# Performance work log

Hardware: AMD Instinct MI355X
Metric: run time of the kernel (lower is better)

The kernel has to match this reference:

```python
import jax, jax.numpy as jnp
import numpy as np

H = 256  # hidden_dim
Z = 4    # z_dim

def gru_step(x, h, Wih, Whh, bih, bhh):
    gi = x @ Wih.T + bih            # [B, 3H]
    gh = h @ Whh.T + bhh            # [B, 3H]
    ir, iz, inn = jnp.split(gi, 3, axis=-1)
    hr, hz, hn = jnp.split(gh, 3, axis=-1)
    r = jax.nn.sigmoid(ir + hr)
    z = jax.nn.sigmoid(iz + hz)
    n = jnp.tanh(inn + r * hn)
    return (1.0 - z) * n + z * h

def gru_scan(xs, h0, Wih, Whh, bih, bhh):
    # xs: [L, B, D] time-major; returns all hidden states [L, B, H]
    def step(h, x):
        h = gru_step(x, h, Wih, Whh, bih, bhh)
        return h, h
    _, hs = jax.lax.scan(step, h0, xs)
    return hs

def feat_z(z, fz_W1, fz_b1, fz_W2, fz_b2):
    # MLPEmbedding(z_dim -> [z_dim//2] -> feature_z), Linear+tanh per layer (dropout off in eval)
    h = jnp.tanh(z @ fz_W1.T + fz_b1)
    return jnp.tanh(h @ fz_W2.T + fz_b2)

def _make_params(key):
    ks = jax.random.split(key, 32)
    s = 0.05
    p = {}
    p['fx_W'] = jax.random.normal(ks[0], (64, 1)) * s
    p['fx_b'] = jnp.zeros((64,))
    p['fz_W1'] = jax.random.normal(ks[1], (2, 4)) * s
    p['fz_b1'] = jnp.zeros((2,))
    p['fz_W2'] = jax.random.normal(ks[2], (32, 2)) * s
    p['fz_b2'] = jnp.zeros((32,))
    p['phi1_Wih'] = jax.random.normal(ks[3], (3 * H, 64)) * s
    p['phi1_Whh'] = jax.random.normal(ks[4], (3 * H, H)) * s
    p['phi1_bih'] = jnp.zeros((3 * H,))
    p['phi1_bhh'] = jnp.zeros((3 * H,))
    p['phi2_Wih'] = jax.random.normal(ks[5], (3 * H, 32)) * s
    p['phi2_Whh'] = jax.random.normal(ks[6], (3 * H, H)) * s
    p['phi2_bih'] = jnp.zeros((3 * H,))
    p['phi2_bhh'] = jnp.zeros((3 * H,))
    p['pn_locW'] = jax.random.normal(ks[7], (Z, 2 * H)) * s
    p['pn_locb'] = jnp.zeros((Z,))
    p['pn_scaleW'] = jax.random.normal(ks[8], (Z, 2 * H)) * s
    p['pn_scaleb'] = jnp.zeros((Z,))
    p['th_Wih'] = jax.random.normal(ks[9], (3 * H, 32)) * s
    p['th_Whh'] = jax.random.normal(ks[10], (3 * H, H)) * s
    p['th_bih'] = jnp.zeros((3 * H,))
    p['th_bhh'] = jnp.zeros((3 * H,))
    p['tn_locW'] = jax.random.normal(ks[11], (1, H)) * s
    p['tn_locb'] = jnp.zeros((1,))
    return p

def setup_inputs() -> dict:
    key = jax.random.key(0)
    kx, ke, kp = jax.random.split(key, 3)
    B, L = 256, 512
    inp = {
        'x': jax.random.normal(kx, (B, L, 1), dtype=jnp.float32),
        'eps': jax.random.normal(ke, (L, B, Z), dtype=jnp.float32),
    }
    inp.update(_make_params(kp))
    return inp

def reference(x, eps, fx_W, fx_b, fz_W1, fz_b1, fz_W2, fz_b2,
              phi1_Wih, phi1_Whh, phi1_bih, phi1_bhh,
              phi2_Wih, phi2_Whh, phi2_bih, phi2_bhh,
              pn_locW, pn_locb, pn_scaleW, pn_scaleb,
              th_Wih, th_Whh, th_bih, th_bhh,
              tn_locW, tn_locb):
    B, L, _ = x.shape
    # ---- encode ----
    xf = jnp.tanh(x @ fx_W.T + fx_b)                 # [B, L, 64] feature_extra_x
    xs_rev = jnp.transpose(xf[:, ::-1, :], (1, 0, 2))  # [L, B, 64] reversed, time-major
    h0 = jnp.zeros((B, H), dtype=x.dtype)
    xh = gru_scan(xs_rev, h0, phi1_Wih, phi1_Whh, phi1_bih, phi1_bhh)  # [L, B, H]
    xh_r = xh[::-1]                                  # flip back to forward time order

    def enc_step(carry, inp_t):
        zh, zf = carry
        xh_t, eps_t = inp_t
        zh = gru_step(zf, zh, phi2_Wih, phi2_Whh, phi2_bih, phi2_bhh)
        cat = jnp.concatenate([zh, xh_t], axis=-1)   # [B, 2H]
        z_loc = cat @ pn_locW.T + pn_locb
        z_scale = jax.nn.softplus(cat @ pn_scaleW.T + pn_scaleb)
        z_t = z_loc + z_scale * eps_t                # Normal sample (n_sample=1 -> mean == sample)
        zf = feat_z(z_t, fz_W1, fz_b1, fz_W2, fz_b2)
        return (zh, zf), z_t

    zf0 = jnp.zeros((B, 32), dtype=x.dtype)
    _, z_tm = jax.lax.scan(enc_step, (h0, zf0), (xh_r, eps))  # [L, B, Z]

    # ---- decode ----
    zf_seq = feat_z(z_tm, fz_W1, fz_b1, fz_W2, fz_b2)          # [L, B, 32]
    hs = gru_scan(zf_seq, h0, th_Wih, th_Whh, th_bih, th_bhh)  # [L, B, H]
    x_loc = hs @ tn_locW.T + tn_locb                           # [L, B, 1]
    return jnp.transpose(x_loc, (1, 0, 2))                     # [B, L, 1]
```

## Files before the change

### kernel.cpp

```cpp
#include <hip/hip_runtime.h>
#include <hip/hip_bf16.h>
#include <stdint.h>


struct RvaeParams {
  const float *x, *eps;
  const float *fx_W, *fx_b;
  const float *fz_W1, *fz_b1, *fz_W2, *fz_b2;
  const float *p1_Wih, *p1_Whh, *p1_bih, *p1_bhh;
  const float *p2_Wih, *p2_Whh, *p2_bih, *p2_bhh;
  const float *pn_locW, *pn_locb, *pn_scaleW, *pn_scaleb;
  const float *th_Wih, *th_Whh, *th_bih, *th_bhh;
  const float *tn_locW, *tn_locb;
  float* out;
  unsigned* ctr;
  float* hbuf;
  float* zpart;
  float* zf_seq;
  __hip_bfloat16* xh;
};

__device__ __forceinline__ float agent_load_f32(const float* p) {
  return __hip_atomic_load(p, __ATOMIC_RELAXED, __HIP_MEMORY_SCOPE_AGENT);
}
__device__ __forceinline__ void agent_store_f32(float* p, float v) {
  __hip_atomic_store(p, v, __ATOMIC_RELAXED, __HIP_MEMORY_SCOPE_AGENT);
}
__device__ __forceinline__ unsigned long long agent_load_u64(const unsigned long long* p) {
  return __hip_atomic_load(p, __ATOMIC_RELAXED, __HIP_MEMORY_SCOPE_AGENT);
}
__device__ __forceinline__ float sigm(float xx) { return 1.0f / (1.0f + __expf(-xx)); }
__device__ __forceinline__ float ftanh(float xx) { return 1.0f - 2.0f / (__expf(2.0f * xx) + 1.0f); }
__device__ __forceinline__ float softplusf(float xx) { return (xx > 15.0f) ? xx : log1pf(__expf(xx)); }

__device__ __forceinline__ void gh_part(const float* Wh, const float* hL, int b, int u,
                                        float& ar, float& az, float& an) {
  float r0 = 0.f, z0 = 0.f, n0 = 0.f;
  const float4* h4 = (const float4*)hL + b * 65;
  const float4* wr = (const float4*)Wh + u * 65;
  const float4* wz = (const float4*)Wh + (32 + u) * 65;
  const float4* wn = (const float4*)Wh + (64 + u) * 65;
#pragma unroll 4
  for (int k = 0; k < 64; ++k) {
    float4 hv = h4[k];
    float4 a = wr[k]; float4 c = wz[k]; float4 d = wn[k];
    r0 = fmaf(a.x, hv.x, r0); r0 = fmaf(a.y, hv.y, r0); r0 = fmaf(a.z, hv.z, r0); r0 = fmaf(a.w, hv.w, r0);
    z0 = fmaf(c.x, hv.x, z0); z0 = fmaf(c.y, hv.y, z0); z0 = fmaf(c.z, hv.z, z0); z0 = fmaf(c.w, hv.w, z0);
    n0 = fmaf(d.x, hv.x, n0); n0 = fmaf(d.y, hv.y, n0); n0 = fmaf(d.z, hv.z, n0); n0 = fmaf(d.w, hv.w, n0);
  }
  ar = r0; az = z0; an = n0;
}

template<int KD4>
__device__ __forceinline__ void gi_part(const float* Wi, int strideF4, const float* inL, int b, int u,
                                        float& gr, float& gz, float& gn) {
  float r0 = 0.f, z0 = 0.f, n0 = 0.f;
  const float4* i4 = (const float4*)inL + b * 17;
  const float4* wr = (const float4*)Wi + u * strideF4;
  const float4* wz = (const float4*)Wi + (32 + u) * strideF4;
  const float4* wn = (const float4*)Wi + (64 + u) * strideF4;
#pragma unroll 4
  for (int k = 0; k < KD4; ++k) {
    float4 hv = i4[k];
    float4 a = wr[k]; float4 c = wz[k]; float4 d = wn[k];
    r0 = fmaf(a.x, hv.x, r0); r0 = fmaf(a.y, hv.y, r0); r0 = fmaf(a.z, hv.z, r0); r0 = fmaf(a.w, hv.w, r0);
    z0 = fmaf(c.x, hv.x, z0); z0 = fmaf(c.y, hv.y, z0); z0 = fmaf(c.z, hv.z, z0); z0 = fmaf(c.w, hv.w, z0);
    n0 = fmaf(d.x, hv.x, n0); n0 = fmaf(d.y, hv.y, n0); n0 = fmaf(d.z, hv.z, n0); n0 = fmaf(d.w, hv.w, n0);
  }
  gr = r0; gz = z0; gn = n0;
}

extern "C" __global__ void __launch_bounds__(256, 1) rvae_main(RvaeParams P) {
  __shared__ __align__(16) float Wh[96 * 260];
  __shared__ __align__(16) float SB[7584];
  __shared__ __align__(16) float hL[8 * 260];
  __shared__ __align__(16) float inL[8 * 68];
  __shared__ float bihL[96], bhhL[96];
  __shared__ float fxwL[64], fxbL[64];
  __shared__ float fzW1L[8], fzb1L[2], fzW2L[64], fzb2L[32];
  __shared__ float pnlb[4], pnsb[4];
  __shared__ float wred[4 * 8 * 8];
  __shared__ float zred[64];
  __shared__ float ztL[32];
  __shared__ float hmL[16];
  __shared__ float oredL[4 * 8];
  __shared__ float tnwL[32];
  __shared__ unsigned bcount;

  const int tid = threadIdx.x;
  const int wgid = blockIdx.x;
  const int s = wgid >> 5;
  const int g = wgid & 31;
  const int b_l = tid & 7;
  const int u = tid >> 3;
  const int j = s * 32 + u;
  const int bg = g * 8 + b_l;
  unsigned* gctr = P.ctr + g * 16;

  if (tid < 64) { fxwL[tid] = P.fx_W[tid]; fxbL[tid] = P.fx_b[tid]; fzW2L[tid] = P.fz_W2[tid]; }
  if (tid < 8)  fzW1L[tid] = P.fz_W1[tid];
  if (tid < 2)  fzb1L[tid] = P.fz_b1[tid];
  if (tid < 32) fzb2L[tid] = P.fz_b2[tid];
  if (tid < 4)  { pnlb[tid] = P.pn_locb[tid]; pnsb[tid] = P.pn_scaleb[tid]; }
  if (tid == 0) bcount = 0;

  auto gbar = [&]() {
    __syncthreads();
    if (tid == 0) {
      unsigned target = (++bcount) * 8u;
      __hip_atomic_fetch_add(gctr, 1u, __ATOMIC_RELEASE, __HIP_MEMORY_SCOPE_AGENT);
      int guard = 0;
      while (__hip_atomic_load(gctr, __ATOMIC_ACQUIRE, __HIP_MEMORY_SCOPE_AGENT) < target) {
        __builtin_amdgcn_s_sleep(1);
        if (++guard > (1 << 27)) break;
      }
    }
    __syncthreads();
  };

  auto load_whh = [&](const float* Whh) {
    for (int rr = 0; rr < 96; ++rr) {
      int gate = rr >> 5, uu = rr & 31;
      Wh[rr * 260 + tid] = Whh[(gate * 256 + s * 32 + uu) * 256 + tid];
    }
  };
  auto load_wih32 = [&](const float* Wih) {
    for (int blk = 0; blk < 12; ++blk) {
      int rr = blk * 8 + (tid >> 5); int c = tid & 31;
      int gate = rr >> 5, uu = rr & 31;
      SB[rr * 36 + c] = Wih[(gate * 256 + s * 32 + uu) * 32 + c];
    }
  };
  auto load_bias = [&](const float* bih, const float* bhh) {
    if (tid < 96) {
      int gate = tid >> 5, uu = tid & 31;
      bihL[tid] = bih[gate * 256 + s * 32 + uu];
      bhhL[tid] = bhh[gate * 256 + s * 32 + uu];
    }
  };

  load_whh(P.p1_Whh);
  for (int blk = 0; blk < 24; ++blk) {
    int rr = blk * 4 + (tid >> 6); int c = tid & 63;
    int gate = rr >> 5, uu = rr & 31;
    SB[rr * 68 + c] = P.p1_Wih[(gate * 256 + s * 32 + uu) * 64 + c];
  }
  load_bias(P.p1_bih, P.p1_bhh);
  agent_store_f32(P.hbuf + bg * 256 + j, 0.0f);
  {
#pragma unroll
    for (int i = 0; i < 2; ++i) {
      int idx = tid + i * 256; int bb = idx >> 6, k = idx & 63;
      float xv = P.x[(size_t)(g * 8 + bb) * 512 + 511];
      inL[bb * 68 + k] = ftanh(fmaf(xv, fxwL[k], fxbL[k]));
    }
  }
  gbar();
  for (int t = 0; t < 512; ++t) {
    const float* hin = P.hbuf + (t & 1) * 65536 + g * 2048;
    float* hout = P.hbuf + ((t + 1) & 1) * 65536;
    unsigned long long hv[4];
    const unsigned long long* h64 = (const unsigned long long*)hin;
#pragma unroll
    for (int i = 0; i < 4; ++i) hv[i] = agent_load_u64(h64 + tid + i * 256);
    float gr, gz, gn;
    gi_part<16>(SB, 17, inL, b_l, u, gr, gz, gn);
#pragma unroll
    for (int i = 0; i < 4; ++i) {
      int idx = tid + i * 256; int bb = idx >> 7, kp = (idx & 127) * 2;
      union { unsigned long long q; float f[2]; } cv; cv.q = hv[i];
      hL[bb * 260 + kp] = cv.f[0]; hL[bb * 260 + kp + 1] = cv.f[1];
    }
    __syncthreads();
    float ar, az, an;
    gh_part(Wh, hL, b_l, u, ar, az, an);
    float hold = hL[b_l * 260 + j];
    float r = sigm(gr + bihL[u] + ar + bhhL[u]);
    float z = sigm(gz + bihL[32 + u] + az + bhhL[32 + u]);
    float n = ftanh(fmaf(r, an + bhhL[64 + u], gn + bihL[64 + u]));
    float hnew = fmaf(z, hold - n, n);
    int t_in = 511 - t;
    agent_store_f32(hout + bg * 256 + j, hnew);
    P.xh[((size_t)wgid * 512 + t_in) * 256 + b_l * 32 + u] = __float2bfloat16(hnew);
    if (t < 511) {
#pragma unroll
      for (int i = 0; i < 2; ++i) {
        int idx = tid + i * 256; int bb = idx >> 6, k = idx & 63;
        float xv = P.x[(size_t)(g * 8 + bb) * 512 + (t_in - 1)];
        inL[bb * 68 + k] = ftanh(fmaf(xv, fxwL[k], fxbL[k]));
      }
    }
    gbar();
  }

  __syncthreads();
  load_whh(P.p2_Whh);
  load_wih32(P.p2_Wih);
  for (int idx = tid; idx < 2048; idx += 256) {
    int o = idx >> 9, c = idx & 511;
    SB[3456 + o * 516 + c] = P.pn_locW[idx];
    SB[5520 + o * 516 + c] = P.pn_scaleW[idx];
  }
  load_bias(P.p2_bih, P.p2_bhh);
  agent_store_f32(P.hbuf + bg * 256 + j, 0.0f);
  for (int idx = tid; idx < 8 * 68; idx += 256) inL[idx] = 0.0f;
  gbar();
  for (int t = 0; t < 512; ++t) {
    const float* hin = P.hbuf + (t & 1) * 65536 + g * 2048;
    float* hout = P.hbuf + ((t + 1) & 1) * 65536;
    unsigned long long hv[4];
    const unsigned long long* h64 = (const unsigned long long*)hin;
#pragma unroll
    for (int i = 0; i < 4; ++i) hv[i] = agent_load_u64(h64 + tid + i * 256);
    float xhv = __bfloat162float(P.xh[((size_t)wgid * 512 + t) * 256 + b_l * 32 + u]);
    float gr, gz, gn;
    gi_part<8>(SB, 9, inL, b_l, u, gr, gz, gn);
#pragma unroll
    for (int i = 0; i < 4; ++i) {
      int idx = tid + i * 256; int bb = idx >> 7, kp = (idx & 127) * 2;
      union { unsigned long long q; float f[2]; } cv; cv.q = hv[i];
      hL[bb * 260 + kp] = cv.f[0]; hL[bb * 260 + kp + 1] = cv.f[1];
    }
    __syncthreads();
    float ar, az, an;
    gh_part(Wh, hL, b_l, u, ar, az, an);
    float hold = hL[b_l * 260 + j];
    float r = sigm(gr + bihL[u] + ar + bhhL[u]);
    float z = sigm(gz + bihL[32 + u] + az + bhhL[32 + u]);
    float n = ftanh(fmaf(r, an + bhhL[64 + u], gn + bihL[64 + u]));
    float hnew = fmaf(z, hold - n, n);
    agent_store_f32(hout + bg * 256 + j, hnew);
    float p[8];
#pragma unroll
    for (int o = 0; o < 4; ++o)
      p[o] = fmaf(hnew, SB[3456 + o * 516 + j], xhv * SB[3456 + o * 516 + 256 + j]);
#pragma unroll
    for (int o = 0; o < 4; ++o)
      p[4 + o] = fmaf(hnew, SB[5520 + o * 516 + j], xhv * SB[5520 + o * 516 + 256 + j]);
#pragma unroll
    for (int o = 0; o < 8; ++o) {
      float v = p[o];
      v += __shfl_down(v, 32); v += __shfl_down(v, 16); v += __shfl_down(v, 8);
      p[o] = v;
    }
    {
      int lane = tid & 63, wv = tid >> 6;
      if (lane < 8) {
#pragma unroll
        for (int o = 0; o < 8; ++o) wred[wv * 64 + lane * 8 + o] = p[o];
      }
    }
    __syncthreads();
    float* zp = P.zpart + (t & 1) * 16384 + g * 512;
    if (tid < 64) {
      int bb = tid >> 3, o = tid & 7;
      float sum = wred[bb * 8 + o] + wred[64 + bb * 8 + o] + wred[128 + bb * 8 + o] + wred[192 + bb * 8 + o];
      agent_store_f32(zp + s * 64 + bb * 8 + o, sum);
    }
    gbar();
    if (tid < 64) {
      int bb = tid >> 3, o = tid & 7;
      float sum = 0.f;
#pragma unroll
      for (int sp = 0; sp < 8; ++sp) sum += agent_load_f32(zp + sp * 64 + bb * 8 + o);
      zred[bb * 8 + o] = sum;
    }
    __syncthreads();
    if (tid < 32) {
      int bb = tid >> 2, zi = tid & 3;
      float loc = zred[bb * 8 + zi] + pnlb[zi];
      float sc = softplusf(zred[bb * 8 + 4 + zi] + pnsb[zi]);
      float e = P.eps[((size_t)t * 256 + g * 8 + bb) * 4 + zi];
      ztL[bb * 4 + zi] = fmaf(sc, e, loc);
    }
    __syncthreads();
    if (tid < 16) {
      int bb = tid >> 1, m = tid & 1;
      float a = fzb1L[m];
#pragma unroll
      for (int i = 0; i < 4; ++i) a = fmaf(ztL[bb * 4 + i], fzW1L[m * 4 + i], a);
      hmL[bb * 2 + m] = ftanh(a);
    }
    __syncthreads();
    {
      int bb = tid >> 5, o = tid & 31;
      float zf = ftanh(fmaf(hmL[bb * 2], fzW2L[o * 2], fmaf(hmL[bb * 2 + 1], fzW2L[o * 2 + 1], fzb2L[o])));
      inL[bb * 68 + o] = zf;
      if (s == 0) agent_store_f32(P.zf_seq + ((size_t)t * 256 + g * 8 + bb) * 32 + o, zf);
    }
    __syncthreads();
  }

  __syncthreads();
  load_whh(P.th_Whh);
  load_wih32(P.th_Wih);
  load_bias(P.th_bih, P.th_bhh);
  if (tid < 32) tnwL[tid] = P.tn_locW[s * 32 + tid];
  agent_store_f32(P.hbuf + bg * 256 + j, 0.0f);
  gbar();
  const float tnb = P.tn_locb[0];
  for (int t = 0; t < 512; ++t) {
    const float* hin = P.hbuf + (t & 1) * 65536 + g * 2048;
    float* hout = P.hbuf + ((t + 1) & 1) * 65536;
    unsigned long long hv[4];
    const unsigned long long* h64 = (const unsigned long long*)hin;
#pragma unroll
    for (int i = 0; i < 4; ++i) hv[i] = agent_load_u64(h64 + tid + i * 256);
    {
      int bb = tid >> 5, o = tid & 31;
      inL[bb * 68 + o] = agent_load_f32(P.zf_seq + ((size_t)t * 256 + g * 8 + bb) * 32 + o);
    }
#pragma unroll
    for (int i = 0; i < 4; ++i) {
      int idx = tid + i * 256; int bb = idx >> 7, kp = (idx & 127) * 2;
      union { unsigned long long q; float f[2]; } cv; cv.q = hv[i];
      hL[bb * 260 + kp] = cv.f[0]; hL[bb * 260 + kp + 1] = cv.f[1];
    }
    __syncthreads();
    float gr, gz, gn;
    gi_part<8>(SB, 9, inL, b_l, u, gr, gz, gn);
    float ar, az, an;
    gh_part(Wh, hL, b_l, u, ar, az, an);
    float hold = hL[b_l * 260 + j];
    float r = sigm(gr + bihL[u] + ar + bhhL[u]);
    float z = sigm(gz + bihL[32 + u] + az + bhhL[32 + u]);
    float n = ftanh(fmaf(r, an + bhhL[64 + u], gn + bihL[64 + u]));
    float hnew = fmaf(z, hold - n, n);
    agent_store_f32(hout + bg * 256 + j, hnew);
    float pv = hnew * tnwL[u];
    pv += __shfl_down(pv, 32); pv += __shfl_down(pv, 16); pv += __shfl_down(pv, 8);
    {
      int lane = tid & 63, wv = tid >> 6;
      if (lane < 8) oredL[wv * 8 + lane] = pv;
    }
    __syncthreads();
    if (tid < 8) {
      float v = oredL[tid] + oredL[8 + tid] + oredL[16 + tid] + oredL[24 + tid];
      if (s == 0) v += tnb;
      atomicAdd(P.out + (size_t)(g * 8 + tid) * 512 + t, v);
    }
    gbar();
  }
}

extern "C" void kernel_launch(void* const* d_in, const int* in_sizes, int n_in,
                              void* d_out, int out_size, void* d_ws, size_t ws_size,
                              hipStream_t stream) {
  (void)in_sizes; (void)n_in; (void)ws_size;
  RvaeParams P;
  P.x        = (const float*)d_in[0];
  P.eps      = (const float*)d_in[1];
  P.fx_W     = (const float*)d_in[2];  P.fx_b     = (const float*)d_in[3];
  P.fz_W1    = (const float*)d_in[4];  P.fz_b1    = (const float*)d_in[5];
  P.fz_W2    = (const float*)d_in[6];  P.fz_b2    = (const float*)d_in[7];
  P.p1_Wih   = (const float*)d_in[8];  P.p1_Whh   = (const float*)d_in[9];
  P.p1_bih   = (const float*)d_in[10]; P.p1_bhh   = (const float*)d_in[11];
  P.p2_Wih   = (const float*)d_in[12]; P.p2_Whh   = (const float*)d_in[13];
  P.p2_bih   = (const float*)d_in[14]; P.p2_bhh   = (const float*)d_in[15];
  P.pn_locW  = (const float*)d_in[16]; P.pn_locb  = (const float*)d_in[17];
  P.pn_scaleW= (const float*)d_in[18]; P.pn_scaleb= (const float*)d_in[19];
  P.th_Wih   = (const float*)d_in[20]; P.th_Whh   = (const float*)d_in[21];
  P.th_bih   = (const float*)d_in[22]; P.th_bhh   = (const float*)d_in[23];
  P.tn_locW  = (const float*)d_in[24]; P.tn_locb  = (const float*)d_in[25];
  P.out = (float*)d_out;
  char* ws = (char*)d_ws;
  P.ctr    = (unsigned*)ws;
  P.hbuf   = (float*)(ws + 4096);
  P.zpart  = (float*)(ws + 4096 + 524288);
  P.zf_seq = (float*)(ws + 4096 + 524288 + 131072);
  P.xh = (__hip_bfloat16*)(ws + 4096 + 524288 + 131072 + 16777216);

  hipMemsetAsync(d_out, 0, (size_t)out_size * sizeof(float), stream);
  hipMemsetAsync(d_ws, 0, 4096, stream);
  void* args[] = { (void*)&P };
  hipError_t err = hipLaunchCooperativeKernel((void*)rvae_main, dim3(256), dim3(256), args, 0, stream);
  if (err != hipSuccess) {
    hipLaunchKernelGGL(rvae_main, dim3(256), dim3(256), 0, stream, P);
  }
}
```

Before: 12.78 ms.

## Keep GRU recurrent weights in registers with split-K DPP reduction, 512 threads

Moves each block's slice of the recurrent Whh (and Wih) weights out of LDS and into per-thread registers. Each thread now handles 16 input columns for one hidden unit across all 8 batch rows, and the partial sums are combined with DPP row reductions. Blocks grow to 512 threads so the dot-product work is spread over more lanes and LDS weight traffic per step goes away. In exchange it needs a lot of registers per thread, adds a shuffle reduction and an extra LDS stage (gsum) each step, and adds a padding array that looks meant to shape LDS allocation or occupancy.

```diff
diff --git a/kernel.cpp b/kernel.cpp
--- a/kernel.cpp
+++ b/kernel.cpp
@@ -29,80 +29,66 @@
 __device__ __forceinline__ unsigned long long agent_load_u64(const unsigned long long* p) {
   return __hip_atomic_load(p, __ATOMIC_RELAXED, __HIP_MEMORY_SCOPE_AGENT);
 }
-__device__ __forceinline__ float sigm(float xx) { return 1.0f / (1.0f + __expf(-xx)); }
-__device__ __forceinline__ float ftanh(float xx) { return 1.0f - 2.0f / (__expf(2.0f * xx) + 1.0f); }
-__device__ __forceinline__ float softplusf(float xx) { return (xx > 15.0f) ? xx : log1pf(__expf(xx)); }
-
-__device__ __forceinline__ void gh_part(const float* Wh, const float* hL, int b, int u,
-                                        float& ar, float& az, float& an) {
-  float r0 = 0.f, z0 = 0.f, n0 = 0.f;
-  const float4* h4 = (const float4*)hL + b * 65;
-  const float4* wr = (const float4*)Wh + u * 65;
-  const float4* wz = (const float4*)Wh + (32 + u) * 65;
-  const float4* wn = (const float4*)Wh + (64 + u) * 65;
-#pragma unroll 4
-  for (int k = 0; k < 64; ++k) {
-    float4 hv = h4[k];
-    float4 a = wr[k]; float4 c = wz[k]; float4 d = wn[k];
-    r0 = fmaf(a.x, hv.x, r0); r0 = fmaf(a.y, hv.y, r0); r0 = fmaf(a.z, hv.z, r0); r0 = fmaf(a.w, hv.w, r0);
-    z0 = fmaf(c.x, hv.x, z0); z0 = fmaf(c.y, hv.y, z0); z0 = fmaf(c.z, hv.z, z0); z0 = fmaf(c.w, hv.w, z0);
-    n0 = fmaf(d.x, hv.x, n0); n0 = fmaf(d.y, hv.y, n0); n0 = fmaf(d.z, hv.z, n0); n0 = fmaf(d.w, hv.w, n0);
-  }
-  ar = r0; az = z0; an = n0;
-}
-
-template<int KD4>
-__device__ __forceinline__ void gi_part(const float* Wi, int strideF4, const float* inL, int b, int u,
-                                        float& gr, float& gz, float& gn) {
-  float r0 = 0.f, z0 = 0.f, n0 = 0.f;
-  const float4* i4 = (const float4*)inL + b * 17;
-  const float4* wr = (const float4*)Wi + u * strideF4;
-  const float4* wz = (const float4*)Wi + (32 + u) * strideF4;
-  const float4* wn = (const float4*)Wi + (64 + u) * strideF4;
-#pragma unroll 4
-  for (int k = 0; k < KD4; ++k) {
-    float4 hv = i4[k];
-    float4 a = wr[k]; float4 c = wz[k]; float4 d = wn[k];
-    r0 = fmaf(a.x, hv.x, r0); r0 = fmaf(a.y, hv.y, r0); r0 = fmaf(a.z, hv.z, r0); r0 = fmaf(a.w, hv.w, r0);
-    z0 = fmaf(c.x, hv.x, z0); z0 = fmaf(c.y, hv.y, z0); z0 = fmaf(c.z, hv.z, z0); z0 = fmaf(c.w, hv.w, z0);
-    n0 = fmaf(d.x, hv.x, n0); n0 = fmaf(d.y, hv.y, n0); n0 = fmaf(d.z, hv.z, n0); n0 = fmaf(d.w, hv.w, n0);
-  }
-  gr = r0; gz = z0; gn = n0;
-}
-
-extern "C" __global__ void __launch_bounds__(256, 1) rvae_main(RvaeParams P) {
-  __shared__ __align__(16) float Wh[96 * 260];
-  __shared__ __align__(16) float SB[7584];
-  __shared__ __align__(16) float hL[8 * 260];
+__device__ __forceinline__ float sigm(float v) { return 1.0f / (1.0f + __expf(-v)); }
+__device__ __forceinline__ float ftanh(float v) { return 1.0f - 2.0f / (__expf(2.0f * v) + 1.0f); }
+__device__ __forceinline__ float softplusf(float v) { return (v > 15.0f) ? v : log1pf(__expf(v)); }
+
+template<int CTRL>
+__device__ __forceinline__ float dpp_add(float v) {
+  int x = __builtin_amdgcn_update_dpp(0, __float_as_int(v), CTRL, 0xf, 0xf, true);
+  return v + __int_as_float(x);
+}
+__device__ __forceinline__ float row_reduce16(float v) {
+  v = dpp_add<0x111>(v);
+  v = dpp_add<0x112>(v);
+  v = dpp_add<0x114>(v);
+  v = dpp_add<0x118>(v);
+  return v;
+}
+
+extern "C" __global__ void __launch_bounds__(512, 2) rvae_main(RvaeParams P) {
+  __shared__ __align__(16) float hL[8 * 320];
   __shared__ __align__(16) float inL[8 * 68];
+  __shared__ __align__(16) float gsum[8 * 132];
+  __shared__ __align__(16) float SB[2 * 4 * 516];
   __shared__ float bihL[96], bhhL[96];
   __shared__ float fxwL[64], fxbL[64];
   __shared__ float fzW1L[8], fzb1L[2], fzW2L[64], fzb2L[32];
   __shared__ float pnlb[4], pnsb[4];
-  __shared__ float wred[4 * 8 * 8];
+  __shared__ float wred[256];
   __shared__ float zred[64];
   __shared__ float ztL[32];
   __shared__ float hmL[16];
-  __shared__ float oredL[4 * 8];
+  __shared__ float oredL[32];
   __shared__ float tnwL[32];
   __shared__ unsigned bcount;
+  __shared__ float lds_pad[11776];
 
   const int tid = threadIdx.x;
   const int wgid = blockIdx.x;
   const int s = wgid >> 5;
   const int g = wgid & 31;
+  const int kap = tid & 15;
+  const int uu = tid >> 4;
   const int b_l = tid & 7;
-  const int u = tid >> 3;
-  const int j = s * 32 + u;
+  const int up = (tid >> 3) & 31;
+  const int j = s * 32 + up;
   const int bg = g * 8 + b_l;
   unsigned* gctr = P.ctr + g * 16;
 
   if (tid < 64) { fxwL[tid] = P.fx_W[tid]; fxbL[tid] = P.fx_b[tid]; fzW2L[tid] = P.fz_W2[tid]; }
   if (tid < 8)  fzW1L[tid] = P.fz_W1[tid];
   if (tid < 2)  fzb1L[tid] = P.fz_b1[tid];
-  if (tid < 32) fzb2L[tid] = P.fz_b2[tid];
+  if (tid < 32) { fzb2L[tid] = P.fz_b2[tid]; tnwL[tid] = P.tn_locW[s * 32 + tid]; }
   if (tid < 4)  { pnlb[tid] = P.pn_locb[tid]; pnsb[tid] = P.pn_scaleb[tid]; }
   if (tid == 0) bcount = 0;
+  lds_pad[tid] = (float)tid;
+  asm volatile("" : : "v"(lds_pad[tid]) : "memory");
+
+  float whr[16], whz[16], whn[16];
+  float wir[4], wiz[4], win[4];
+  float pr[8], pz[8], pni[8], pnh[8];
+  unsigned long long q0, q1;
 
   auto gbar = [&]() {
     __syncthreads();
@@ -118,132 +104,183 @@
     __syncthreads();
   };
 
-  auto load_whh = [&](const float* Whh) {
-    for (int rr = 0; rr < 96; ++rr) {
-      int gate = rr >> 5, uu = rr & 31;
-      Wh[rr * 260 + tid] = Whh[(gate * 256 + s * 32 + uu) * 256 + tid];
-    }
-  };
-  auto load_wih32 = [&](const float* Wih) {
-    for (int blk = 0; blk < 12; ++blk) {
-      int rr = blk * 8 + (tid >> 5); int c = tid & 31;
-      int gate = rr >> 5, uu = rr & 31;
-      SB[rr * 36 + c] = Wih[(gate * 256 + s * 32 + uu) * 32 + c];
-    }
+  auto load_whh_regs = [&](const float* Whh) {
+    const float* base = Whh + (size_t)(s * 32 + uu) * 256 + kap * 16;
+#pragma unroll
+    for (int c = 0; c < 4; ++c) {
+      float4 vr = *(const float4*)(base + c * 4);
+      float4 vz = *(const float4*)(base + 65536 + c * 4);
+      float4 vn = *(const float4*)(base + 131072 + c * 4);
+      whr[4*c+0]=vr.x; whr[4*c+1]=vr.y; whr[4*c+2]=vr.z; whr[4*c+3]=vr.w;
+      whz[4*c+0]=vz.x; whz[4*c+1]=vz.y; whz[4*c+2]=vz.z; whz[4*c+3]=vz.w;
+      whn[4*c+0]=vn.x; whn[4*c+1]=vn.y; whn[4*c+2]=vn.z; whn[4*c+3]=vn.w;
+    }
+  };
+  auto load_wih64_regs = [&](const float* Wih) {
+    const float* base = Wih + (size_t)(s * 32 + uu) * 64 + kap * 4;
+    float4 vr = *(const float4*)(base);
+    float4 vz = *(const float4*)(base + 16384);
+    float4 vn = *(const float4*)(base + 32768);
+    wir[0]=vr.x; wir[1]=vr.y; wir[2]=vr.z; wir[3]=vr.w;
+    wiz[0]=vz.x; wiz[1]=vz.y; wiz[2]=vz.z; wiz[3]=vz.w;
+    win[0]=vn.x; win[1]=vn.y; win[2]=vn.z; win[3]=vn.w;
+  };
+  auto load_wih32_regs = [&](const float* Wih) {
+    const float* base = Wih + (size_t)(s * 32 + uu) * 32 + kap * 2;
+    float2 vr = *(const float2*)(base);
+    float2 vz = *(const float2*)(base + 8192);
+    float2 vn = *(const float2*)(base + 16384);
+    wir[0]=vr.x; wir[1]=vr.y; wiz[0]=vz.x; wiz[1]=vz.y; win[0]=vn.x; win[1]=vn.y;
   };
   auto load_bias = [&](const float* bih, const float* bhh) {
     if (tid < 96) {
-      int gate = tid >> 5, uu = tid & 31;
-      bihL[tid] = bih[gate * 256 + s * 32 + uu];
-      bhhL[tid] = bhh[gate * 256 + s * 32 + uu];
-    }
-  };
-
-  load_whh(P.p1_Whh);
-  for (int blk = 0; blk < 24; ++blk) {
-    int rr = blk * 4 + (tid >> 6); int c = tid & 63;
-    int gate = rr >> 5, uu = rr & 31;
-    SB[rr * 68 + c] = P.p1_Wih[(gate * 256 + s * 32 + uu) * 64 + c];
-  }
+      int gate = tid >> 5, u2 = tid & 31;
+      bihL[tid] = bih[gate * 256 + s * 32 + u2];
+      bhhL[tid] = bhh[gate * 256 + s * 32 + u2];
+    }
+  };
+  auto load_h_issue = [&](int t) {
+    const unsigned long long* h64 =
+        (const unsigned long long*)(P.hbuf + (t & 1) * 65536 + g * 2048) + tid * 2;
+    q0 = agent_load_u64(h64);
+    q1 = agent_load_u64(h64 + 1);
+  };
+  auto stage_h = [&]() {
+    int bb = tid >> 6, k4 = tid & 63;
+    union { unsigned long long q[2]; float f[4]; } cv; cv.q[0] = q0; cv.q[1] = q1;
+    float* dst = hL + bb * 320 + (k4 >> 2) * 20 + (k4 & 3) * 4;
+    *(float4*)dst = make_float4(cv.f[0], cv.f[1], cv.f[2], cv.f[3]);
+  };
+  auto gh_accum = [&]() {
+#pragma unroll
+    for (int b = 0; b < 8; ++b) {
+      const float* hp = hL + b * 320 + kap * 20;
+      float4 hcv[4];
+      hcv[0] = *(const float4*)(hp);     hcv[1] = *(const float4*)(hp + 4);
+      hcv[2] = *(const float4*)(hp + 8); hcv[3] = *(const float4*)(hp + 12);
+      float r = pr[b], z = pz[b], n = pnh[b];
+#pragma unroll
+      for (int c = 0; c < 4; ++c) {
+        r = fmaf(whr[4*c+0], hcv[c].x, r); r = fmaf(whr[4*c+1], hcv[c].y, r);
+        r = fmaf(whr[4*c+2], hcv[c].z, r); r = fmaf(whr[4*c+3], hcv[c].w, r);
+        z = fmaf(whz[4*c+0], hcv[c].x, z); z = fmaf(whz[4*c+1], hcv[c].y, z);
+        z = fmaf(whz[4*c+2], hcv[c].z, z); z = fmaf(whz[4*c+3], hcv[c].w, z);
+        n = fmaf(whn[4*c+0], hcv[c].x, n); n = fmaf(whn[4*c+1], hcv[c].y, n);
+        n = fmaf(whn[4*c+2], hcv[c].z, n); n = fmaf(whn[4*c+3], hcv[c].w, n);
+      }
+      pr[b] = r; pz[b] = z; pnh[b] = n;
+    }
+  };
+  auto reduce_write = [&]() {
+#pragma unroll
+    for (int b = 0; b < 8; ++b) {
+      pr[b] = row_reduce16(pr[b]);  pz[b] = row_reduce16(pz[b]);
+      pni[b] = row_reduce16(pni[b]); pnh[b] = row_reduce16(pnh[b]);
+    }
+    if (kap == 15) {
+#pragma unroll
+      for (int b = 0; b < 8; ++b) {
+        gsum[b*132 + uu]      = pr[b];
+        gsum[b*132 + 32 + uu] = pz[b];
+        gsum[b*132 + 64 + uu] = pni[b];
+        gsum[b*132 + 96 + uu] = pnh[b];
+      }
+    }
+  };
+  auto pointwise_h = [&](int t) -> float {
+    float rr = sigm(gsum[b_l*132 + up]      + bihL[up]      + bhhL[up]);
+    float zz = sigm(gsum[b_l*132 + 32 + up] + bihL[32 + up] + bhhL[32 + up]);
+    float nn = ftanh(fmaf(rr, gsum[b_l*132 + 96 + up] + bhhL[64 + up],
+                              gsum[b_l*132 + 64 + up] + bihL[64 + up]));
+    float hold = hL[b_l*320 + ((j >> 4) * 20) + (j & 15)];
+    float hnew = fmaf(zz, hold - nn, nn);
+    agent_store_f32(P.hbuf + (((t + 1) & 1) * 65536) + bg * 256 + j, hnew);
+    return hnew;
+  };
+
+  load_whh_regs(P.p1_Whh);
+  load_wih64_regs(P.p1_Wih);
   load_bias(P.p1_bih, P.p1_bhh);
-  agent_store_f32(P.hbuf + bg * 256 + j, 0.0f);
+  if (tid < 256) agent_store_f32(P.hbuf + bg * 256 + j, 0.0f);
+  __syncthreads();
   {
-#pragma unroll
-    for (int i = 0; i < 2; ++i) {
-      int idx = tid + i * 256; int bb = idx >> 6, k = idx & 63;
-      float xv = P.x[(size_t)(g * 8 + bb) * 512 + 511];
+    int bb = tid >> 6, k = tid & 63;
+    float xv = P.x[(size_t)(g * 8 + bb) * 512 + 511];
+    inL[bb * 68 + k] = ftanh(fmaf(xv, fxwL[k], fxbL[k]));
+  }
+  gbar();
+#pragma unroll 1
+  for (int t = 0; t < 512; ++t) {
+    load_h_issue(t);
+#pragma unroll
+    for (int b = 0; b < 8; ++b) {
+      float4 iv = *(const float4*)(inL + b * 68 + kap * 4);
+      pr[b]  = fmaf(wir[0], iv.x, fmaf(wir[1], iv.y, fmaf(wir[2], iv.z, wir[3] * iv.w)));
+      pz[b]  = fmaf(wiz[0], iv.x, fmaf(wiz[1], iv.y, fmaf(wiz[2], iv.z, wiz[3] * iv.w)));
+      pni[b] = fmaf(win[0], iv.x, fmaf(win[1], iv.y, fmaf(win[2], iv.z, win[3] * iv.w)));
+      pnh[b] = 0.0f;
+    }
+    stage_h();
+    __syncthreads();
+    gh_accum();
+    reduce_write();
+    __syncthreads();
+    int t_in = 511 - t;
+    if (tid < 256) {
+      float hnew = pointwise_h(t);
+      P.xh[((size_t)wgid * 512 + t_in) * 256 + b_l * 32 + up] = __float2bfloat16(hnew);
+    }
+    if (t < 511) {
+      int bb = tid >> 6, k = tid & 63;
+      float xv = P.x[(size_t)(g * 8 + bb) * 512 + (t_in - 1)];
       inL[bb * 68 + k] = ftanh(fmaf(xv, fxwL[k], fxbL[k]));
     }
-  }
+    gbar();
+  }
+
+  load_whh_regs(P.p2_Whh);
+  load_wih32_regs(P.p2_Wih);
+  load_bias(P.p2_bih, P.p2_bhh);
+  for (int idx = tid; idx < 2048; idx += 512) {
+    int o = idx >> 9, c = idx & 511;
+    SB[o * 516 + c] = P.pn_locW[idx];
+    SB[2064 + o * 516 + c] = P.pn_scaleW[idx];
+  }
+  if (tid < 256) agent_store_f32(P.hbuf + bg * 256 + j, 0.0f);
+  for (int idx = tid; idx < 8 * 36; idx += 512) inL[idx] = 0.0f;
   gbar();
+#pragma unroll 1
   for (int t = 0; t < 512; ++t) {
-    const float* hin = P.hbuf + (t & 1) * 65536 + g * 2048;
-    float* hout = P.hbuf + ((t + 1) & 1) * 65536;
-    unsigned long long hv[4];
-    const unsigned long long* h64 = (const unsigned long long*)hin;
-#pragma unroll
-    for (int i = 0; i < 4; ++i) hv[i] = agent_load_u64(h64 + tid + i * 256);
-    float gr, gz, gn;
-    gi_part<16>(SB, 17, inL, b_l, u, gr, gz, gn);
-#pragma unroll
-    for (int i = 0; i < 4; ++i) {
-      int idx = tid + i * 256; int bb = idx >> 7, kp = (idx & 127) * 2;
-      union { unsigned long long q; float f[2]; } cv; cv.q = hv[i];
-      hL[bb * 260 + kp] = cv.f[0]; hL[bb * 260 + kp + 1] = cv.f[1];
-    }
-    __syncthreads();
-    float ar, az, an;
-    gh_part(Wh, hL, b_l, u, ar, az, an);
-    float hold = hL[b_l * 260 + j];
-    float r = sigm(gr + bihL[u] + ar + bhhL[u]);
-    float z = sigm(gz + bihL[32 + u] + az + bhhL[32 + u]);
-    float n = ftanh(fmaf(r, an + bhhL[64 + u], gn + bihL[64 + u]));
-    float hnew = fmaf(z, hold - n, n);
-    int t_in = 511 - t;
-    agent_store_f32(hout + bg * 256 + j, hnew);
-    P.xh[((size_t)wgid * 512 + t_in) * 256 + b_l * 32 + u] = __float2bfloat16(hnew);
-    if (t < 511) {
-#pragma unroll
-      for (int i = 0; i < 2; ++i) {
-        int idx = tid + i * 256; int bb = idx >> 6, k = idx & 63;
-        float xv = P.x[(size_t)(g * 8 + bb) * 512 + (t_in - 1)];
-        inL[bb * 68 + k] = ftanh(fmaf(xv, fxwL[k], fxbL[k]));
+    load_h_issue(t);
+#pragma unroll
+    for (int b = 0; b < 8; ++b) {
+      float2 iv = *(const float2*)(inL + b * 36 + kap * 2);
+      pr[b]  = fmaf(wir[0], iv.x, wir[1] * iv.y);
+      pz[b]  = fmaf(wiz[0], iv.x, wiz[1] * iv.y);
+      pni[b] = fmaf(win[0], iv.x, win[1] * iv.y);
+      pnh[b] = 0.0f;
+    }
+    stage_h();
+    __syncthreads();
+    gh_accum();
+    reduce_write();
+    __syncthreads();
+    if (tid < 256) {
+      float hnew = pointwise_h(t);
+      float xhv = __bfloat162float(P.xh[((size_t)wgid * 512 + t) * 256 + b_l * 32 + up]);
+      float p[8];
+#pragma unroll
+      for (int o = 0; o < 4; ++o)
+        p[o] = fmaf(hnew, SB[o * 516 + j], xhv * SB[o * 516 + 256 + j]);
+#pragma unroll
+      for (int o = 0; o < 4; ++o)
+        p[4 + o] = fmaf(hnew, SB[2064 + o * 516 + j], xhv * SB[2064 + o * 516 + 256 + j]);
+#pragma unroll
+      for (int o = 0; o < 8; ++o) {
+        float v = p[o];
+        v += __shfl_down(v, 32); v += __shfl_down(v, 16); v += __shfl_down(v, 8);
+        p[o] = v;
       }
-    }
-    gbar();
-  }
-
-  __syncthreads();
-  load_whh(P.p2_Whh);
-  load_wih32(P.p2_Wih);
-  for (int idx = tid; idx < 2048; idx += 256) {
-    int o = idx >> 9, c = idx & 511;
-    SB[3456 + o * 516 + c] = P.pn_locW[idx];
-    SB[5520 + o * 516 + c] = P.pn_scaleW[idx];
-  }
-  load_bias(P.p2_bih, P.p2_bhh);
-  agent_store_f32(P.hbuf + bg * 256 + j, 0.0f);
-  for (int idx = tid; idx < 8 * 68; idx += 256) inL[idx] = 0.0f;
-  gbar();
-  for (int t = 0; t < 512; ++t) {
-    const float* hin = P.hbuf + (t & 1) * 65536 + g * 2048;
-    float* hout = P.hbuf + ((t + 1) & 1) * 65536;
-    unsigned long long hv[4];
-    const unsigned long long* h64 = (const unsigned long long*)hin;
-#pragma unroll
-    for (int i = 0; i < 4; ++i) hv[i] = agent_load_u64(h64 + tid + i * 256);
-    float xhv = __bfloat162float(P.xh[((size_t)wgid * 512 + t) * 256 + b_l * 32 + u]);
-    float gr, gz, gn;
-    gi_part<8>(SB, 9, inL, b_l, u, gr, gz, gn);
-#pragma unroll
-    for (int i = 0; i < 4; ++i) {
-      int idx = tid + i * 256; int bb = idx >> 7, kp = (idx & 127) * 2;
-      union { unsigned long long q; float f[2]; } cv; cv.q = hv[i];
-      hL[bb * 260 + kp] = cv.f[0]; hL[bb * 260 + kp + 1] = cv.f[1];
-    }
-    __syncthreads();
-    float ar, az, an;
-    gh_part(Wh, hL, b_l, u, ar, az, an);
-    float hold = hL[b_l * 260 + j];
-    float r = sigm(gr + bihL[u] + ar + bhhL[u]);
-    float z = sigm(gz + bihL[32 + u] + az + bhhL[32 + u]);
-    float n = ftanh(fmaf(r, an + bhhL[64 + u], gn + bihL[64 + u]));
-    float hnew = fmaf(z, hold - n, n);
-    agent_store_f32(hout + bg * 256 + j, hnew);
-    float p[8];
-#pragma unroll
-    for (int o = 0; o < 4; ++o)
-      p[o] = fmaf(hnew, SB[3456 + o * 516 + j], xhv * SB[3456 + o * 516 + 256 + j]);
-#pragma unroll
-    for (int o = 0; o < 4; ++o)
-      p[4 + o] = fmaf(hnew, SB[5520 + o * 516 + j], xhv * SB[5520 + o * 516 + 256 + j]);
-#pragma unroll
-    for (int o = 0; o < 8; ++o) {
-      float v = p[o];
-      v += __shfl_down(v, 32); v += __shfl_down(v, 16); v += __shfl_down(v, 8);
-      p[o] = v;
-    }
-    {
       int lane = tid & 63, wv = tid >> 6;
       if (lane < 8) {
 #pragma unroll
@@ -254,7 +291,7 @@
     float* zp = P.zpart + (t & 1) * 16384 + g * 512;
     if (tid < 64) {
       int bb = tid >> 3, o = tid & 7;
-      float sum = wred[bb * 8 + o] + wred[64 + bb * 8 + o] + wred[128 + bb * 8 + o] + wred[192 + bb * 8 + o];
+      float sum = wred[bb*8+o] + wred[64+bb*8+o] + wred[128+bb*8+o] + wred[192+bb*8+o];
       agent_store_f32(zp + s * 64 + bb * 8 + o, sum);
     }
     gbar();
@@ -282,54 +319,47 @@
       hmL[bb * 2 + m] = ftanh(a);
     }
     __syncthreads();
-    {
+    if (tid < 256) {
       int bb = tid >> 5, o = tid & 31;
-      float zf = ftanh(fmaf(hmL[bb * 2], fzW2L[o * 2], fmaf(hmL[bb * 2 + 1], fzW2L[o * 2 + 1], fzb2L[o])));
-      inL[bb * 68 + o] = zf;
+      float zf = ftanh(fmaf(hmL[bb * 2], fzW2L[o * 2],
+                       fmaf(hmL[bb * 2 + 1], fzW2L[o * 2 + 1], fzb2L[o])));
+      inL[bb * 36 + o] = zf;
       if (s == 0) agent_store_f32(P.zf_seq + ((size_t)t * 256 + g * 8 + bb) * 32 + o, zf);
     }
     __syncthreads();
   }
 
-  __syncthreads();
-  load_whh(P.th_Whh);
-  load_wih32(P.th_Wih);
+  load_whh_regs(P.th_Whh);
+  load_wih32_regs(P.th_Wih);
   load_bias(P.th_bih, P.th_bhh);
-  if (tid < 32) tnwL[tid] = P.tn_locW[s * 32 + tid];
-  agent_store_f32(P.hbuf + bg * 256 + j, 0.0f);
+  if (tid < 256) agent_store_f32(P.hbuf + bg * 256 + j, 0.0f);
   gbar();
   const float tnb = P.tn_locb[0];
+#pragma unroll 1
   for (int t = 0; t < 512; ++t) {
-    const float* hin = P.hbuf + (t & 1) * 65536 + g * 2048;
-    float* hout = P.hbuf + ((t + 1) & 1) * 65536;
-    unsigned long long hv[4];
-    const unsigned long long* h64 = (const unsigned long long*)hin;
-#pragma unroll
-    for (int i = 0; i < 4; ++i) hv[i] = agent_load_u64(h64 + tid + i * 256);
-    {
-      int bb = tid >> 5, o = tid & 31;
-      inL[bb * 68 + o] = agent_load_f32(P.zf_seq + ((size_t)t * 256 + g * 8 + bb) * 32 + o);
-    }
-#pragma unroll
-    for (int i = 0; i < 4; ++i) {
-      int idx = tid + i * 256; int bb = idx >> 7, kp = (idx & 127) * 2;
-      union { unsigned long long q; float f[2]; } cv; cv.q = hv[i];
-      hL[bb * 260 + kp] = cv.f[0]; hL[bb * 260 + kp + 1] = cv.f[1];
-    }
-    __syncthreads();
-    float gr, gz, gn;
-    gi_part<8>(SB, 9, inL, b_l, u, gr, gz, gn);
-    float ar, az, an;
-    gh_part(Wh, hL, b_l, u, ar, az, an);
-    float hold = hL[b_l * 260 + j];
-    float r = sigm(gr + bihL[u] + ar + bhhL[u]);
-    float z = sigm(gz + bihL[32 + u] + az + bhhL[32 + u]);
-    float n = ftanh(fmaf(r, an + bhhL[64 + u], gn + bihL[64 + u]));
-    float hnew = fmaf(z, hold - n, n);
-    agent_store_f32(hout + bg * 256 + j, hnew);
-    float pv = hnew * tnwL[u];
-    pv += __shfl_down(pv, 32); pv += __shfl_down(pv, 16); pv += __shfl_down(pv, 8);
-    {
+    load_h_issue(t);
+    unsigned long long zq[8];
+#pragma unroll
+    for (int b = 0; b < 8; ++b)
+      zq[b] = agent_load_u64((const unsigned long long*)P.zf_seq +
+                             ((size_t)t * 256 + g * 8 + b) * 16 + kap);
+#pragma unroll
+    for (int b = 0; b < 8; ++b) {
+      union { unsigned long long q; float f[2]; } zc; zc.q = zq[b];
+      pr[b]  = fmaf(wir[0], zc.f[0], wir[1] * zc.f[1]);
+      pz[b]  = fmaf(wiz[0], zc.f[0], wiz[1] * zc.f[1]);
+      pni[b] = fmaf(win[0], zc.f[0], win[1] * zc.f[1]);
+      pnh[b] = 0.0f;
+    }
+    stage_h();
+    __syncthreads();
+    gh_accum();
+    reduce_write();
+    __syncthreads();
+    if (tid < 256) {
+      float hnew = pointwise_h(t);
+      float pv = hnew * tnwL[up];
+      pv += __shfl_down(pv, 32); pv += __shfl_down(pv, 16); pv += __shfl_down(pv, 8);
       int lane = tid & 63, wv = tid >> 6;
       if (lane < 8) oredL[wv * 8 + lane] = pv;
     }
@@ -373,8 +403,8 @@
   hipMemsetAsync(d_out, 0, (size_t)out_size * sizeof(float), stream);
   hipMemsetAsync(d_ws, 0, 4096, stream);
   void* args[] = { (void*)&P };
-  hipError_t err = hipLaunchCooperativeKernel((void*)rvae_main, dim3(256), dim3(256), args, 0, stream);
+  hipError_t err = hipLaunchCooperativeKernel((void*)rvae_main, dim3(256), dim3(512), args, 0, stream);
   if (err != hipSuccess) {
-    hipLaunchKernelGGL(rvae_main, dim3(256), dim3(256), 0, stream, P);
-  }
-}
+    hipLaunchKernelGGL(rvae_main, dim3(256), dim3(512), 0, stream, P);
+  }
+}
```

Measured after the change: 11.68 ms. 1.09x faster.
